# Kernel optimization log

Measured on AMD Instinct MI355X. Metric: run time of the kernel, lower is better.

The kernel has to match this reference:

```python
import math
import jax, jax.numpy as jnp
import numpy as np

B, T, D = 8, 2048, 512


def setup_inputs() -> dict:
    key = jax.random.key(0)
    kx, = jax.random.split(key, 1)
    x = jax.random.normal(kx, (B, T, D), dtype=jnp.float32)
    log_tau = jnp.asarray(math.log(2.0), dtype=jnp.float32)
    log_blend = jnp.asarray(math.log(0.3 / 0.7), dtype=jnp.float32)
    return {"x": x, "log_tau": log_tau, "log_blend": log_blend}


def _gelu_tanh(x):
    c = math.sqrt(2.0 / math.pi)
    return 0.5 * x * (1.0 + jnp.tanh(c * (x + 0.044715 * x * x * x)))


def reference(x, log_tau, log_blend):
    Bb, Tt, Dd = x.shape
    tau = jnp.exp(log_tau)
    alpha = jax.nn.sigmoid(log_blend)
    # F.normalize(x, dim=-1): divide by L2 norm clamped to eps=1e-12
    norm = jnp.maximum(jnp.linalg.norm(x, axis=-1, keepdims=True), 1e-12)
    x_norm = x / norm
    # cosine self-similarity [B, T, T]
    sim = jnp.einsum("btd,bsd->bts", x_norm, x_norm)
    # triu(diagonal=0) masks j >= i (current + future positions)
    causal_mask = jnp.triu(jnp.ones((Tt, Tt), dtype=bool), k=0)
    sim_causal = jnp.where(causal_mask[None, :, :], -jnp.inf, sim)
    max_sim = jnp.max(sim_causal, axis=-1)  # [B, T]; row 0 is -inf
    max_sim = jnp.nan_to_num(max_sim, nan=0.0, posinf=1.0, neginf=-1.0)
    novelty = jnp.exp(-tau * max_sim)
    scale = (1.0 - alpha + alpha * novelty)[..., None]  # [B, T, 1]
    return _gelu_tanh(x * scale)
```

## Files before the change

### kernel.cpp

```cpp
#include <hip/hip_runtime.h>

#define B_ 8
#define T_ 2048
#define D_ 512
#define BT 128
#define BK 64
#define NT (T_/BT)
#define NTILES (NT*(NT+1)/2)

typedef float f32x4 __attribute__((ext_vector_type(4)));
typedef __bf16 bf16x8 __attribute__((ext_vector_type(8)));

__device__ __forceinline__ unsigned encf(float f) {
    int i = __float_as_int(f);
    return (i < 0) ? ~((unsigned)i) : (((unsigned)i) | 0x80000000u);
}
__device__ __forceinline__ float decf(unsigned u) {
    unsigned b = (u & 0x80000000u) ? (u ^ 0x80000000u) : ~u;
    return __int_as_float((int)b);
}

__device__ __forceinline__ void gload_lds16(const __bf16* g, __bf16* l) {
    __builtin_amdgcn_global_load_lds(
        (const __attribute__((address_space(1))) unsigned int*)g,
        (__attribute__((address_space(3))) unsigned int*)l, 16, 0, 0);
}

__global__ __launch_bounds__(256) void rownorm_kernel(
        const float* __restrict__ x, __bf16* __restrict__ xn,
        unsigned* __restrict__ msim) {
    int row  = blockIdx.x * 4 + (threadIdx.x >> 6);
    int lane = threadIdx.x & 63;
    const float* p = x + (size_t)row * D_ + lane * 8;
    float4 a = *(const float4*)p;
    float4 b = *(const float4*)(p + 4);
    float ss = a.x*a.x + a.y*a.y + a.z*a.z + a.w*a.w
             + b.x*b.x + b.y*b.y + b.z*b.z + b.w*b.w;
#pragma unroll
    for (int m = 32; m; m >>= 1) ss += __shfl_xor(ss, m);
    float r = 1.0f / fmaxf(sqrtf(ss), 1e-12f);
    bf16x8 h;
    h[0] = (__bf16)(a.x * r); h[1] = (__bf16)(a.y * r);
    h[2] = (__bf16)(a.z * r); h[3] = (__bf16)(a.w * r);
    h[4] = (__bf16)(b.x * r); h[5] = (__bf16)(b.y * r);
    h[6] = (__bf16)(b.z * r); h[7] = (__bf16)(b.w * r);
    *(bf16x8*)(xn + (size_t)row * D_ + lane * 8) = h;
    if (lane == 0) msim[row] = 0x407FFFFFu;
}

__global__ __launch_bounds__(256, 4) void simmax_kernel(
        const __bf16* __restrict__ xn, unsigned* __restrict__ msim) {
    __shared__ __attribute__((aligned(16))) __bf16 sA[BT * BK];
    __shared__ __attribute__((aligned(16))) __bf16 sB[BT * BK];

    int bid = blockIdx.x;
    int b   = bid & 7;
    int s   = bid >> 3;
    int it  = 0;
    while ((it + 1) * (it + 2) / 2 <= s) it++;
    int jt  = s - it * (it + 1) / 2;

    int tid  = threadIdx.x;
    int lane = tid & 63;
    int w    = tid >> 6;
    int wr   = w >> 1;
    int wc   = w & 1;
    int fr   = lane & 15;
    int kg   = lane >> 4;

    const size_t rowA0 = (size_t)b * T_ + (size_t)it * BT;
    const size_t rowB0 = (size_t)b * T_ + (size_t)jt * BT;

    int rb   = lane >> 3;
    int csrc = (lane & 7) ^ rb;
    const __bf16* gA0 = xn + (rowA0 + w * 32 + rb) * D_ + csrc * 8;
    const __bf16* gB0 = xn + (rowB0 + w * 32 + rb) * D_ + csrc * 8;
    __bf16* lA0 = sA + (w * 32) * BK;
    __bf16* lB0 = sB + (w * 32) * BK;

    f32x4 acc[4][4];
#pragma unroll
    for (int m = 0; m < 4; m++)
#pragma unroll
        for (int n = 0; n < 4; n++)
            acc[m][n] = (f32x4){0.f, 0.f, 0.f, 0.f};

    int swz = (fr & 7) << 4;
    int laA = (wr * 64 + fr) * 128 + kg * 16;
    int laB = (wc * 64 + fr) * 128 + kg * 16;

    for (int kc = 0; kc < D_ / BK; kc++) {
        int k0 = kc * BK;
        __syncthreads();
#pragma unroll
        for (int p = 0; p < 4; p++) {
            gload_lds16(gA0 + (size_t)p * 8 * D_ + k0, lA0 + p * 8 * BK);
            gload_lds16(gB0 + (size_t)p * 8 * D_ + k0, lB0 + p * 8 * BK);
        }
        __syncthreads();
#pragma unroll
        for (int ks = 0; ks < 2; ks++) {
            bf16x8 af[4], bfr[4];
#pragma unroll
            for (int n = 0; n < 4; n++)
                bfr[n] = *(const bf16x8*)((const char*)sB +
                           ((laB + n * 16 * 128 + ks * 64) ^ swz));
#pragma unroll
            for (int m = 0; m < 4; m++)
                af[m] = *(const bf16x8*)((const char*)sA +
                           ((laA + m * 16 * 128 + ks * 64) ^ swz));
#pragma unroll
            for (int m = 0; m < 4; m++)
#pragma unroll
                for (int n = 0; n < 4; n++)
                    acc[m][n] = __builtin_amdgcn_mfma_f32_16x16x32_bf16(
                        af[m], bfr[n], acc[m][n], 0, 0, 0);
        }
    }

    bool diag = (it == jt);
    unsigned* mrow = msim + (size_t)b * T_ + (size_t)it * BT;
    const float NINF = -__builtin_inff();
#pragma unroll
    for (int m = 0; m < 4; m++) {
#pragma unroll
        for (int e = 0; e < 4; e++) {
            int rloc = wr * 64 + m * 16 + kg * 4 + e;
            float v = NINF;
#pragma unroll
            for (int n = 0; n < 4; n++) {
                int cloc = wc * 64 + n * 16 + fr;
                float t = acc[m][n][e];
                if (diag && cloc >= rloc) t = NINF;
                v = fmaxf(v, t);
            }
            v = fmaxf(v, __shfl_xor(v, 1));
            v = fmaxf(v, __shfl_xor(v, 2));
            v = fmaxf(v, __shfl_xor(v, 4));
            v = fmaxf(v, __shfl_xor(v, 8));
            if (fr == 0) atomicMax(&mrow[rloc], encf(v));
        }
    }
}

__global__ __launch_bounds__(256) void gelu_kernel(
        const float* __restrict__ x, const unsigned* __restrict__ msim,
        const float* __restrict__ ltau, const float* __restrict__ lblend,
        float* __restrict__ out) {
    int i = blockIdx.x * 256 + threadIdx.x;
    float tau   = __expf(ltau[0]);
    float alpha = 1.f / (1.f + __expf(-lblend[0]));
    int row = i >> 7;
    float ms = decf(msim[row]);
    float sc = (1.f - alpha) + alpha * __expf(-tau * ms);
    float4 v = ((const float4*)x)[i];
    const float c0 = 0.7978845608028654f;
    const float c1 = 0.044715f;
    float4 o;
#pragma unroll
    for (int j = 0; j < 4; j++) {
        float z = ((const float*)&v)[j] * sc;
        float u = c0 * (z + c1 * z * z * z);
        float t = __expf(2.f * u);
        float th = 1.f - 2.f / (t + 1.f);
        ((float*)&o)[j] = 0.5f * z * (1.f + th);
    }
    ((float4*)out)[i] = o;
}

extern "C" void kernel_launch(void* const* d_in, const int* in_sizes, int n_in,
                              void* d_out, int out_size, void* d_ws, size_t ws_size,
                              hipStream_t stream) {
    (void)in_sizes; (void)n_in; (void)out_size; (void)ws_size;
    const float* x      = (const float*)d_in[0];
    const float* ltau   = (const float*)d_in[1];
    const float* lblend = (const float*)d_in[2];
    float*    out   = (float*)d_out;
    __bf16*   xn    = (__bf16*)d_out;
    unsigned* msim  = (unsigned*)d_ws;

    rownorm_kernel<<<B_ * T_ / 4, 256, 0, stream>>>(x, xn, msim);
    simmax_kernel<<<B_ * NTILES, 256, 0, stream>>>(xn, msim);
    gelu_kernel<<<(B_ * T_ * D_ / 4) / 256, 256, 0, stream>>>(x, msim, ltau, lblend, out);
}
```

Before: 57.91 us.

## Double-buffer LDS tiles in simmax and skip B loads on diagonal tiles

```diff
diff --git a/kernel.cpp b/kernel.cpp
--- a/kernel.cpp
+++ b/kernel.cpp
@@ -48,10 +48,10 @@
     if (lane == 0) msim[row] = 0x407FFFFFu;
 }
 
-__global__ __launch_bounds__(256, 4) void simmax_kernel(
+__global__ __launch_bounds__(256, 2) void simmax_kernel(
         const __bf16* __restrict__ xn, unsigned* __restrict__ msim) {
-    __shared__ __attribute__((aligned(16))) __bf16 sA[BT * BK];
-    __shared__ __attribute__((aligned(16))) __bf16 sB[BT * BK];
+    __shared__ __attribute__((aligned(16))) __bf16 sA[2][BT * BK];
+    __shared__ __attribute__((aligned(16))) __bf16 sB[2][BT * BK];
 
     int bid = blockIdx.x;
     int b   = bid & 7;
@@ -59,6 +59,7 @@
     int it  = 0;
     while ((it + 1) * (it + 2) / 2 <= s) it++;
     int jt  = s - it * (it + 1) / 2;
+    const bool diag = (it == jt);
 
     int tid  = threadIdx.x;
     int lane = tid & 63;
@@ -75,8 +76,6 @@
     int csrc = (lane & 7) ^ rb;
     const __bf16* gA0 = xn + (rowA0 + w * 32 + rb) * D_ + csrc * 8;
     const __bf16* gB0 = xn + (rowB0 + w * 32 + rb) * D_ + csrc * 8;
-    __bf16* lA0 = sA + (w * 32) * BK;
-    __bf16* lB0 = sB + (w * 32) * BK;
 
     f32x4 acc[4][4];
 #pragma unroll
@@ -89,26 +88,33 @@
     int laA = (wr * 64 + fr) * 128 + kg * 16;
     int laB = (wc * 64 + fr) * 128 + kg * 16;
 
-    for (int kc = 0; kc < D_ / BK; kc++) {
+    auto stage = [&](int buf, int kc) {
         int k0 = kc * BK;
-        __syncthreads();
 #pragma unroll
         for (int p = 0; p < 4; p++) {
-            gload_lds16(gA0 + (size_t)p * 8 * D_ + k0, lA0 + p * 8 * BK);
-            gload_lds16(gB0 + (size_t)p * 8 * D_ + k0, lB0 + p * 8 * BK);
+            gload_lds16(gA0 + (size_t)p * 8 * D_ + k0,
+                        &sA[buf][(w * 32 + p * 8) * BK]);
+            if (!diag)
+                gload_lds16(gB0 + (size_t)p * 8 * D_ + k0,
+                            &sB[buf][(w * 32 + p * 8) * BK]);
         }
-        __syncthreads();
+    };
+
+    auto compute = [&](int buf) {
+        const char* bA = (const char*)&sA[buf][0];
+        const char* bB = diag ? (const char*)&sA[buf][0]
+                              : (const char*)&sB[buf][0];
 #pragma unroll
         for (int ks = 0; ks < 2; ks++) {
             bf16x8 af[4], bfr[4];
 #pragma unroll
             for (int n = 0; n < 4; n++)
-                bfr[n] = *(const bf16x8*)((const char*)sB +
-                           ((laB + n * 16 * 128 + ks * 64) ^ swz));
+                bfr[n] = *(const bf16x8*)(bB +
+                           ((laB + n * 2048 + ks * 64) ^ swz));
 #pragma unroll
             for (int m = 0; m < 4; m++)
-                af[m] = *(const bf16x8*)((const char*)sA +
-                           ((laA + m * 16 * 128 + ks * 64) ^ swz));
+                af[m] = *(const bf16x8*)(bA +
+                           ((laA + m * 2048 + ks * 64) ^ swz));
 #pragma unroll
             for (int m = 0; m < 4; m++)
 #pragma unroll
@@ -116,9 +122,17 @@
                     acc[m][n] = __builtin_amdgcn_mfma_f32_16x16x32_bf16(
                         af[m], bfr[n], acc[m][n], 0, 0, 0);
         }
+    };
+
+    stage(0, 0);
+    __syncthreads();
+    for (int kc = 0; kc < D_ / BK; kc++) {
+        int cur = kc & 1;
+        if (kc < D_ / BK - 1) stage(cur ^ 1, kc + 1);
+        compute(cur);
+        __syncthreads();
     }
 
-    bool diag = (it == jt);
     unsigned* mrow = msim + (size_t)b * T_ + (size_t)it * BT;
     const float NINF = -__builtin_inff();
 #pragma unroll
```

Result: slower. 63.15 us (+9.1%).

## Replace LDS-tiled simmax with single-wave 128x64 tiles loading MFMA operands from global

Applied to the files above, without the earlier changes.

```diff
diff --git a/kernel.cpp b/kernel.cpp
--- a/kernel.cpp
+++ b/kernel.cpp
@@ -3,12 +3,9 @@
 #define B_ 8
 #define T_ 2048
 #define D_ 512
-#define BT 128
-#define BK 64
-#define NT (T_/BT)
-#define NTILES (NT*(NT+1)/2)
+#define NTPB 272
 
-typedef float f32x4 __attribute__((ext_vector_type(4)));
+typedef float f32x16 __attribute__((ext_vector_type(16)));
 typedef __bf16 bf16x8 __attribute__((ext_vector_type(8)));
 
 __device__ __forceinline__ unsigned encf(float f) {
@@ -18,12 +15,6 @@
 __device__ __forceinline__ float decf(unsigned u) {
     unsigned b = (u & 0x80000000u) ? (u ^ 0x80000000u) : ~u;
     return __int_as_float((int)b);
-}
-
-__device__ __forceinline__ void gload_lds16(const __bf16* g, __bf16* l) {
-    __builtin_amdgcn_global_load_lds(
-        (const __attribute__((address_space(1))) unsigned int*)g,
-        (__attribute__((address_space(3))) unsigned int*)l, 16, 0, 0);
 }
 
 __global__ __launch_bounds__(256) void rownorm_kernel(
@@ -48,97 +39,85 @@
     if (lane == 0) msim[row] = 0x407FFFFFu;
 }
 
-__global__ __launch_bounds__(256, 4) void simmax_kernel(
+__global__ __launch_bounds__(64, 2) void simmax_kernel(
         const __bf16* __restrict__ xn, unsigned* __restrict__ msim) {
-    __shared__ __attribute__((aligned(16))) __bf16 sA[BT * BK];
-    __shared__ __attribute__((aligned(16))) __bf16 sB[BT * BK];
-
     int bid = blockIdx.x;
     int b   = bid & 7;
-    int s   = bid >> 3;
-    int it  = 0;
-    while ((it + 1) * (it + 2) / 2 <= s) it++;
-    int jt  = s - it * (it + 1) / 2;
+    int t   = bid >> 3;
+    int i = 0;
+    while ((i + 1) * (i + 2) <= t) i++;
+    int j = t - i * (i + 1);
+    const bool strad = (j >= 2 * i);
 
-    int tid  = threadIdx.x;
-    int lane = tid & 63;
-    int w    = tid >> 6;
-    int wr   = w >> 1;
-    int wc   = w & 1;
-    int fr   = lane & 15;
-    int kg   = lane >> 4;
+    int ln = threadIdx.x;
+    int lr = ln & 31;
+    int hc = ln >> 5;
 
-    const size_t rowA0 = (size_t)b * T_ + (size_t)it * BT;
-    const size_t rowB0 = (size_t)b * T_ + (size_t)jt * BT;
+    const char* xb = (const char*)xn;
+    unsigned baseA = ((unsigned)(b * T_ + i * 128 + lr) * D_ + hc * 8) * 2;
+    unsigned baseB = ((unsigned)(b * T_ + j * 64  + lr) * D_ + hc * 8) * 2;
 
-    int rb   = lane >> 3;
-    int csrc = (lane & 7) ^ rb;
-    const __bf16* gA0 = xn + (rowA0 + w * 32 + rb) * D_ + csrc * 8;
-    const __bf16* gB0 = xn + (rowB0 + w * 32 + rb) * D_ + csrc * 8;
-    __bf16* lA0 = sA + (w * 32) * BK;
-    __bf16* lB0 = sB + (w * 32) * BK;
+    f32x16 acc[4][2];
+#pragma unroll
+    for (int mi = 0; mi < 4; mi++)
+#pragma unroll
+        for (int ni = 0; ni < 2; ni++)
+#pragma unroll
+            for (int r = 0; r < 16; r++)
+                acc[mi][ni][r] = 0.f;
 
-    f32x4 acc[4][4];
+    bf16x8 a[2][4][2], bb[2][2][2];
+
+#define LOADG(buf, g) do {                                                  \
+    _Pragma("unroll")                                                       \
+    for (int mi = 0; mi < 4; mi++) {                                        \
+        a[buf][mi][0] = *(const bf16x8*)(xb + baseA + mi * 32768 + (g) * 64);      \
+        a[buf][mi][1] = *(const bf16x8*)(xb + baseA + mi * 32768 + (g) * 64 + 32); \
+    }                                                                       \
+    _Pragma("unroll")                                                       \
+    for (int ni = 0; ni < 2; ni++) {                                        \
+        bb[buf][ni][0] = *(const bf16x8*)(xb + baseB + ni * 32768 + (g) * 64);      \
+        bb[buf][ni][1] = *(const bf16x8*)(xb + baseB + ni * 32768 + (g) * 64 + 32); \
+    }                                                                       \
+} while (0)
+
+    LOADG(0, 0);
 #pragma unroll
-    for (int m = 0; m < 4; m++)
+    for (int g = 0; g < 16; g++) {
+        if (g < 15) LOADG((g + 1) & 1, g + 1);
 #pragma unroll
-        for (int n = 0; n < 4; n++)
-            acc[m][n] = (f32x4){0.f, 0.f, 0.f, 0.f};
+        for (int h = 0; h < 2; h++)
+#pragma unroll
+            for (int mi = 0; mi < 4; mi++)
+#pragma unroll
+                for (int ni = 0; ni < 2; ni++)
+                    acc[mi][ni] = __builtin_amdgcn_mfma_f32_32x32x16_bf16(
+                        a[g & 1][mi][h], bb[g & 1][ni][h], acc[mi][ni], 0, 0, 0);
+    }
+#undef LOADG
 
-    int swz = (fr & 7) << 4;
-    int laA = (wr * 64 + fr) * 128 + kg * 16;
-    int laB = (wc * 64 + fr) * 128 + kg * 16;
-
-    for (int kc = 0; kc < D_ / BK; kc++) {
-        int k0 = kc * BK;
-        __syncthreads();
+    unsigned* mbase = msim + (size_t)b * T_ + (size_t)i * 128;
+    const float NINF = -__builtin_inff();
+    int gcol0 = j * 64 + lr;
 #pragma unroll
-        for (int p = 0; p < 4; p++) {
-            gload_lds16(gA0 + (size_t)p * 8 * D_ + k0, lA0 + p * 8 * BK);
-            gload_lds16(gB0 + (size_t)p * 8 * D_ + k0, lB0 + p * 8 * BK);
-        }
-        __syncthreads();
+    for (int mi = 0; mi < 4; mi++) {
 #pragma unroll
-        for (int ks = 0; ks < 2; ks++) {
-            bf16x8 af[4], bfr[4];
-#pragma unroll
-            for (int n = 0; n < 4; n++)
-                bfr[n] = *(const bf16x8*)((const char*)sB +
-                           ((laB + n * 16 * 128 + ks * 64) ^ swz));
-#pragma unroll
-            for (int m = 0; m < 4; m++)
-                af[m] = *(const bf16x8*)((const char*)sA +
-                           ((laA + m * 16 * 128 + ks * 64) ^ swz));
-#pragma unroll
-            for (int m = 0; m < 4; m++)
-#pragma unroll
-                for (int n = 0; n < 4; n++)
-                    acc[m][n] = __builtin_amdgcn_mfma_f32_16x16x32_bf16(
-                        af[m], bfr[n], acc[m][n], 0, 0, 0);
-        }
-    }
-
-    bool diag = (it == jt);
-    unsigned* mrow = msim + (size_t)b * T_ + (size_t)it * BT;
-    const float NINF = -__builtin_inff();
-#pragma unroll
-    for (int m = 0; m < 4; m++) {
-#pragma unroll
-        for (int e = 0; e < 4; e++) {
-            int rloc = wr * 64 + m * 16 + kg * 4 + e;
-            float v = NINF;
-#pragma unroll
-            for (int n = 0; n < 4; n++) {
-                int cloc = wc * 64 + n * 16 + fr;
-                float t = acc[m][n][e];
-                if (diag && cloc >= rloc) t = NINF;
-                v = fmaxf(v, t);
+        for (int r = 0; r < 16; r++) {
+            int rloc = mi * 32 + (r & 3) + 8 * (r >> 2) + 4 * hc;
+            int grow = i * 128 + rloc;
+            float t0 = acc[mi][0][r];
+            float t1 = acc[mi][1][r];
+            if (strad) {
+                if (gcol0      >= grow) t0 = NINF;
+                if (gcol0 + 32 >= grow) t1 = NINF;
             }
+            float v = fmaxf(t0, t1);
             v = fmaxf(v, __shfl_xor(v, 1));
             v = fmaxf(v, __shfl_xor(v, 2));
             v = fmaxf(v, __shfl_xor(v, 4));
             v = fmaxf(v, __shfl_xor(v, 8));
-            if (fr == 0) atomicMax(&mrow[rloc], encf(v));
+            v = fmaxf(v, __shfl_xor(v, 16));
+            if (lr == 0) atomicMax(&mbase[rloc], encf(v));
         }
     }
 }
@@ -158,12 +137,12 @@
     const float c1 = 0.044715f;
     float4 o;
 #pragma unroll
-    for (int j = 0; j < 4; j++) {
-        float z = ((const float*)&v)[j] * sc;
+    for (int k = 0; k < 4; k++) {
+        float z = ((const float*)&v)[k] * sc;
         float u = c0 * (z + c1 * z * z * z);
-        float t = __expf(2.f * u);
-        float th = 1.f - 2.f / (t + 1.f);
-        ((float*)&o)[j] = 0.5f * z * (1.f + th);
+        float e = __expf(2.f * u);
+        float th = 1.f - 2.f / (e + 1.f);
+        ((float*)&o)[k] = 0.5f * z * (1.f + th);
     }
     ((float4*)out)[i] = o;
 }
@@ -180,6 +159,6 @@
     unsigned* msim  = (unsigned*)d_ws;
 
     rownorm_kernel<<<B_ * T_ / 4, 256, 0, stream>>>(x, xn, msim);
-    simmax_kernel<<<B_ * NTILES, 256, 0, stream>>>(xn, msim);
+    simmax_kernel<<<B_ * NTPB, 64, 0, stream>>>(xn, msim);
     gelu_kernel<<<(B_ * T_ * D_ / 4) / 256, 256, 0, stream>>>(x, msim, ltau, lblend, out);
 }
```

Result: slower. 95.70 us (+65.3%).
